# Optimization experiments

Hardware: AMD Instinct MI355X
Metric: run time of the kernel (lower is better)

## Reference

```python
import jax, jax.numpy as jnp
import numpy as np

T, D_ENC, H, D_EMB, VOCAB = 4000, 1024, 1024, 512, 8192
V = VOCAB + 1  # + blank
P = 800
TEMPERATURE = 1.0


def setup_inputs() -> dict:
    key = jax.random.key(0)
    ks = jax.random.split(key, 8)
    s = lambda d: 1.0 / np.sqrt(d)
    return {
        'enc_out': jax.random.normal(ks[0], (T, D_ENC), jnp.float32),
        'embedding': jax.random.normal(ks[1], (V, D_EMB), jnp.float32) * s(D_EMB),
        'W_ih': jax.random.normal(ks[2], (4 * H, D_EMB), jnp.float32) * s(D_EMB),
        'W_hh': jax.random.normal(ks[3], (4 * H, H), jnp.float32) * s(H),
        'b_lstm': jnp.zeros((4 * H,), jnp.float32),
        'W_pred': jax.random.normal(ks[4], (D_ENC, H), jnp.float32) * s(H),
        'b_pred': jnp.zeros((D_ENC,), jnp.float32),
        'W_join': jax.random.normal(ks[5], (V, D_ENC), jnp.float32) * s(D_ENC),
        'b_join': jnp.zeros((V,), jnp.float32),
        'phonemes': jax.random.randint(ks[6], (P,), 0, VOCAB, jnp.int32),
    }


def reference(enc_out, embedding, W_ih, W_hh, b_lstm, W_pred, b_pred, W_join, b_join, phonemes):
    blank_idx = embedding.shape[0] - 1
    n_phon = phonemes.shape[0]

    def predict_step(tok, h, c):
        # one-token RNNT predictor: embed -> LSTM cell -> projection to joiner dim
        x = embedding[tok]
        gates = x @ W_ih.T + h @ W_hh.T + b_lstm  # [4H]
        i, f, g, o = jnp.split(gates, 4)
        i, f, o = jax.nn.sigmoid(i), jax.nn.sigmoid(f), jax.nn.sigmoid(o)
        c2 = f * c + i * jnp.tanh(g)
        h2 = o * jnp.tanh(c2)
        pred = h2 @ W_pred.T + b_pred  # [D_ENC]
        return pred, h2, c2

    def step(carry, enc_t):
        tok, h, c, tp = carry
        pred, h2, c2 = predict_step(tok, h, c)
        logits = (jax.nn.relu(enc_t + pred) @ W_join.T + b_join) / TEMPERATURE
        logp = jax.nn.log_softmax(logits)  # [V]
        pick = jnp.argmax(logp)
        phon_done = tp >= n_phon
        is_blank = (pick == blank_idx) | phon_done
        next_phon = phonemes[jnp.minimum(tp, n_phon - 1)]
        prediction = jnp.where(is_blank, blank_idx, next_phon)
        # blank: keep hypothesis token/state; non-blank: advance to phoneme + new state
        tok2 = jnp.where(is_blank, tok, next_phon)
        h3 = jnp.where(is_blank, h, h2)
        c3 = jnp.where(is_blank, c, c2)
        tp2 = tp + jnp.where(is_blank, 0, 1)
        return (tok2, h3, c3, tp2), (logp, prediction, ~phon_done)

    # initial predictor pass with blank token from zero state (mirrors the warm-up predict call)
    h0 = jnp.zeros((W_hh.shape[1],), enc_out.dtype)
    c0 = jnp.zeros_like(h0)
    _, h_init, c_init = predict_step(jnp.int32(blank_idx), h0, c0)
    carry0 = (jnp.int32(blank_idx), h_init, c_init, jnp.int32(0))
    _, (alignment, predictions, valid) = jax.lax.scan(step, carry0, enc_out)
    return alignment, predictions, valid
```

## Files before the change

### kernel.cpp

```cpp
#include <hip/hip_runtime.h>
#include <math.h>

#define TT     4000
#define DENC   1024
#define HD     1024
#define DEMB   512
#define VD     8193
#define NPH    800
#define BLANK  8192
#define NWG    256
#define NTHR   512
#define CHUNK_M 800
#define NSTEP  (NPH + 2)
#define NSTEPP 802
#define NVT    65
#define NP     129
#define CHUNK  256

typedef __bf16 bf16x4 __attribute__((ext_vector_type(4)));
typedef __bf16 bf16x8 __attribute__((ext_vector_type(8)));
typedef float  f32x16 __attribute__((ext_vector_type(16)));

#define MEMSET_BYTES 20480
#define WSF_HX     1024
#define WSF_HHIST  5120
#define WSF_PREDS  826368
#define WSF_GXT    826368
#define WSF_PMAX   1646592
#define WSF_PSUM   2162592
#define WSF_PARG   2678592
#define WSF_LSE    3194592
#define WSF_AMAX   3198592
#define WSF_XBF    3199616
#define WSF_W16    4903552
#define WSF_END    9163392
#define NEED_MFMA  ((size_t)WSF_END * 4)
#define TST_IDX    512

#define L_HX     1024
#define L_HHIST  5120
#define L_PREDS  826368
#define F_PMAX 1646592
#define F_PSUM 1906592
#define F_PARG 2166592
#define F_LSE  2426592

#define GEMM_SMEM  12800
#define CHAIN_SMEM ((16 * NSTEPP + 2048 + 64) * 4)
#define JOIN_SMEM  (65536 + 128)
#define S_XH   0
#define S_GS   3072
#define S_C4   3088
#define S_TOK  3264
#define S_RED  4066
#define S_AMAX 4082
#define SMEM_FLOATS_F32 4352
#define SMEM_BYTES_F32 (SMEM_FLOATS_F32 * 4)


__device__ __forceinline__ float dot4(float4 a, float4 b, float acc) {
  acc = fmaf(a.x, b.x, acc); acc = fmaf(a.y, b.y, acc);
  acc = fmaf(a.z, b.z, acc); acc = fmaf(a.w, b.w, acc);
  return acc;
}
__device__ __forceinline__ float sigmf(float x) { return 1.f / (1.f + expf(-x)); }
__device__ __forceinline__ float sigm_fast(float x) { return 1.f / (1.f + __expf(-x)); }
__device__ __forceinline__ float tanh_fast(float x) {
  float e = __expf(2.f * x);
  return 1.f - 2.f / (e + 1.f);
}

__device__ __forceinline__ void combine3(float& m, float& s, int& am,
                                         float om, float os, int oa) {
  float mm = fmaxf(m, om);
  s = s * __expf(m - mm) + os * __expf(om - mm);
  if (om > m || (om == m && oa < am)) am = oa;
  m = mm;
}

__device__ __forceinline__ void gload16(const void* g, void* l) {
  __builtin_amdgcn_global_load_lds(
      (const __attribute__((address_space(1))) unsigned int*)g,
      (__attribute__((address_space(3))) unsigned int*)l, 16, 0, 0);
}

__device__ __forceinline__ float ld_coh(const float* p) {
  return __hip_atomic_load((const float*)p, __ATOMIC_RELAXED, __HIP_MEMORY_SCOPE_AGENT);
}

__device__ __forceinline__ void light_barrier(unsigned* flags, unsigned& ep) {
  unsigned* arrive  = flags;
  unsigned* release = flags + 256;
  __builtin_amdgcn_s_waitcnt(0);
  __syncthreads();
  if (blockIdx.x == 0) {
    int tid = threadIdx.x;
    if (tid > 0 && tid < NWG) {
      while (__hip_atomic_load(&arrive[tid], __ATOMIC_RELAXED, __HIP_MEMORY_SCOPE_AGENT) != ep) {}
    }
    __syncthreads();
    if (tid == 0)
      __hip_atomic_store(release, ep, __ATOMIC_RELAXED, __HIP_MEMORY_SCOPE_AGENT);
  } else {
    if (threadIdx.x == 0) {
      __hip_atomic_store(&arrive[blockIdx.x], ep, __ATOMIC_RELAXED, __HIP_MEMORY_SCOPE_AGENT);
      while (__hip_atomic_load(release, __ATOMIC_RELAXED, __HIP_MEMORY_SCOPE_AGENT) != ep) {}
    }
    __syncthreads();
  }
  asm volatile("" ::: "memory");
  ep++;
}

__device__ __forceinline__ void heavy_barrier(unsigned* flags) {
  unsigned* bar = flags + 257;
  __syncthreads();
  if (threadIdx.x == 0) {
    __threadfence();
    unsigned g = __hip_atomic_load(&bar[1], __ATOMIC_RELAXED, __HIP_MEMORY_SCOPE_AGENT);
    unsigned v = __hip_atomic_fetch_add(&bar[0], 1u, __ATOMIC_RELAXED, __HIP_MEMORY_SCOPE_AGENT);
    if (v == (unsigned)(NWG - 1)) {
      __hip_atomic_store(&bar[0], 0u, __ATOMIC_RELAXED, __HIP_MEMORY_SCOPE_AGENT);
      __hip_atomic_store(&bar[1], g + 1u, __ATOMIC_RELEASE, __HIP_MEMORY_SCOPE_AGENT);
    } else {
      while (__hip_atomic_load(&bar[1], __ATOMIC_RELAXED, __HIP_MEMORY_SCOPE_AGENT) == g)
        __builtin_amdgcn_s_sleep(1);
    }
    __threadfence();
  }
  __syncthreads();
}

__device__ void xbf_fill(const float* enc, const float* preds, __bf16* dst,
                         int t0, int K, int pi0, int g0, int gs) {
  int total = K << 8;
  for (int q = g0; q < total; q += gs) {
    int j = q >> 8, seg = q & 255;
    int pi = (pi0 < 0) ? NPH : pi0 + j;
    float4 e = ((const float4*)(enc + (size_t)(t0 + j) * 1024))[seg];
    float4 p = ((const float4*)(preds + (size_t)pi * 1024))[seg];
    bf16x4 r;
    r[0] = (__bf16)fmaxf(e.x + p.x, 0.f);
    r[1] = (__bf16)fmaxf(e.y + p.y, 0.f);
    r[2] = (__bf16)fmaxf(e.z + p.z, 0.f);
    r[3] = (__bf16)fmaxf(e.w + p.w, 0.f);
    *(bf16x4*)(dst + (size_t)j * 1024 + (seg << 2)) = r;
  }
}

__device__ void joiner_tiles(const __bf16* W16, const __bf16* xrows, const float* bj,
                             float* out_align, float* pmax, float* psum, int* parg,
                             char* smc, int t0, int K, int tile0, int tstride) {
  const int tid = threadIdx.x;
  const int wid = tid >> 6, lane = tid & 63;
  const int wj = wid & 3, wv = wid >> 2;
  const int l31 = lane & 31, lhi = lane >> 5;
  const int jt_n = (K + 127) >> 7;
  const int ntiles = jt_n * NVT;

  for (int tile = tile0; tile < ntiles; tile += tstride) {
    const int vt = tile % NVT, jt = tile / NVT;
    const int v0 = vt << 7, j0 = jt << 7;
    f32x16 acc0, acc1;
    #pragma unroll
    for (int i = 0; i < 16; ++i) { acc0[i] = 0.f; acc1[i] = 0.f; }

    auto stage = [&](int db, int kb) {
      char* wb = smc + db * 32768;
      char* xb = wb + 16384;
      #pragma unroll
      for (int p = 0; p < 2; ++p) {
        int sbase = p * 512 + wid * 64;
        int s = sbase + lane;
        int ks = s >> 7, r = s & 127;
        gload16(W16 + (size_t)(v0 + r) * 1024 + kb + ks * 8, wb + sbase * 16);
        gload16(xrows + (size_t)(j0 + r) * 1024 + kb + ks * 8, xb + sbase * 16);
      }
    };

    stage(0, 0);
    __syncthreads();
    int db = 0;
    for (int kb16 = 0; kb16 < 16; ++kb16) {
      if (kb16 < 15) stage(db ^ 1, (kb16 + 1) << 6);
      const char* wb = smc + db * 32768;
      const char* xb = wb + 16384;
      #pragma unroll
      for (int k16 = 0; k16 < 4; ++k16) {
        int ks = k16 * 2 + lhi;
        bf16x8 a  = *(const bf16x8*)(xb + ((ks << 7) + (wj << 5) + l31) * 16);
        bf16x8 b0 = *(const bf16x8*)(wb + ((ks << 7) + (wv << 6) + l31) * 16);
        bf16x8 b1 = *(const bf16x8*)(wb + ((ks << 7) + (wv << 6) + 32 + l31) * 16);
        acc0 = __builtin_amdgcn_mfma_f32_32x32x16_bf16(a, b0, acc0, 0, 0, 0);
        acc1 = __builtin_amdgcn_mfma_f32_32x32x16_bf16(a, b1, acc1, 0, 0, 0);
      }
      __syncthreads();
      db ^= 1;
    }

    const int v_0 = v0 + (wv << 6) + l31;
    const int v_1 = v_0 + 32;
    const float bj0 = (v_0 < VD) ? bj[v_0] : 0.f;
    const float bj1 = (v_1 < VD) ? bj[v_1] : 0.f;
    const int jbase = j0 + (wj << 5) + 4 * lhi;
    const bool npok = (v0 + (wv << 6)) < VD;
    const int np = (v0 >> 6) + wv;
    #pragma unroll
    for (int reg = 0; reg < 16; ++reg) {
      int j = jbase + (reg & 3) + 8 * (reg >> 2);
      bool jok = j < K;
      float lg0 = acc0[reg] + bj0;
      float lg1 = acc1[reg] + bj1;
      if (jok) {
        size_t ro = (size_t)(t0 + j) * VD;
        if (v_0 < VD) out_align[ro + v_0] = lg0;
        if (v_1 < VD) out_align[ro + v_1] = lg1;
      }
      float l0 = (v_0 < VD) ? lg0 : -1e30f;
      float l1 = (v_1 < VD) ? lg1 : -1e30f;
      float m = fmaxf(l0, l1);
      float ss = 0.f;
      if (v_0 < VD) ss += __expf(l0 - m);
      if (v_1 < VD) ss += __expf(l1 - m);
      int am = (l1 > l0) ? v_1 : v_0;
      #pragma unroll
      for (int msk = 1; msk <= 16; msk <<= 1) {
        float om = __shfl_xor(m, msk, 64);
        float os = __shfl_xor(ss, msk, 64);
        int oa = __shfl_xor(am, msk, 64);
        float mm = fmaxf(m, om);
        ss = ss * __expf(m - mm) + os * __expf(om - mm);
        if (om > m || (om == m && oa < am)) am = oa;
        m = mm;
      }
      if (l31 == 0 && jok && npok) {
        size_t pb = (size_t)(t0 + j) * NP + np;
        __hip_atomic_store(&pmax[pb], m, __ATOMIC_RELAXED, __HIP_MEMORY_SCOPE_AGENT);
        __hip_atomic_store(&psum[pb], ss, __ATOMIC_RELAXED, __HIP_MEMORY_SCOPE_AGENT);
        __hip_atomic_store(&parg[pb], am, __ATOMIC_RELAXED, __HIP_MEMORY_SCOPE_AGENT);
      }
    }
  }
}

__device__ __forceinline__ void merge_row129(const float* pmax, const float* psum,
                                             const int* parg, int row, int lane,
                                             float& m, float& s, int& am) {
  size_t b = (size_t)row * NP;
  m = ld_coh(pmax + b + lane);
  s = ld_coh(psum + b + lane);
  am = __hip_atomic_load(&parg[b + lane], __ATOMIC_RELAXED, __HIP_MEMORY_SCOPE_AGENT);
  {
    int i2 = lane + 64;
    float om = ld_coh(pmax + b + i2);
    float os = ld_coh(psum + b + i2);
    int oa = __hip_atomic_load(&parg[b + i2], __ATOMIC_RELAXED, __HIP_MEMORY_SCOPE_AGENT);
    combine3(m, s, am, om, os, oa);
  }
  if (lane == 0) {
    float om = ld_coh(pmax + b + 128);
    float os = ld_coh(psum + b + 128);
    int oa = __hip_atomic_load(&parg[b + 128], __ATOMIC_RELAXED, __HIP_MEMORY_SCOPE_AGENT);
    combine3(m, s, am, om, os, oa);
  }
  #pragma unroll
  for (int msk = 32; msk; msk >>= 1) {
    float om = __shfl_xor(m, msk, 64);
    float os = __shfl_xor(s, msk, 64);
    int oa = __shfl_xor(am, msk, 64);
    combine3(m, s, am, om, os, oa);
  }
}

__global__ __launch_bounds__(512) void wconv_kernel(const float* __restrict__ Wjoin,
                                                    float* wsf) {
  __bf16* w16 = (__bf16*)(wsf + WSF_W16);
  int g0 = blockIdx.x * 512 + threadIdx.x;
  int gs = gridDim.x * 512;
  for (int q = g0; q < VD * 256; q += gs) {
    int v = q >> 8, seg = q & 255;
    float4 w4 = ((const float4*)(Wjoin + (size_t)v * 1024))[seg];
    bf16x4 r;
    r[0] = (__bf16)w4.x; r[1] = (__bf16)w4.y; r[2] = (__bf16)w4.z; r[3] = (__bf16)w4.w;
    *(bf16x4*)(w16 + (size_t)v * 1024 + (seg << 2)) = r;
  }
}

__global__ __launch_bounds__(512) void gx_kernel(
    const float* __restrict__ Wih, const float* __restrict__ emb,
    const float* __restrict__ bl, const int* __restrict__ phon, float* wsf) {
  extern __shared__ float sm[];
  float* Wt = sm;
  float* Xt = sm + 2112;
  float* gxT = wsf + WSF_GXT;
  const int tid = threadIdx.x;
  const int tx = tid & 31, ty = tid >> 5;
  int ntiles = 32 * 13;
  for (int tile = blockIdx.x; tile < ntiles; tile += gridDim.x) {
    int vt = tile & 31, jt = tile >> 5;
    int v0 = vt * 128, j0 = jt * 64;
    float acc[4][4];
    #pragma unroll
    for (int a = 0; a < 4; ++a)
      #pragma unroll
      for (int q = 0; q < 4; ++q) acc[a][q] = 0.f;
    for (int kk = 0; kk < DEMB; kk += 16) {
      {
        int r = tid >> 2, seg = tid & 3;
        float4 wv = ((const float4*)(Wih + (size_t)(v0 + r) * DEMB + kk))[seg];
        Wt[(seg * 4 + 0) * 132 + r] = wv.x;
        Wt[(seg * 4 + 1) * 132 + r] = wv.y;
        Wt[(seg * 4 + 2) * 132 + r] = wv.z;
        Wt[(seg * 4 + 3) * 132 + r] = wv.w;
      }
      if (tid < 256) {
        int r = tid >> 2, seg = tid & 3;
        int j = j0 + r;
        float4 xv = make_float4(0.f, 0.f, 0.f, 0.f);
        if (j < NSTEP) {
          int tok = (j < 2) ? BLANK : phon[j - 2];
          xv = ((const float4*)(emb + (size_t)tok * DEMB + kk))[seg];
        }
        Xt[(seg * 4 + 0) * 68 + r] = xv.x;
        Xt[(seg * 4 + 1) * 68 + r] = xv.y;
        Xt[(seg * 4 + 2) * 68 + r] = xv.z;
        Xt[(seg * 4 + 3) * 68 + r] = xv.w;
      }
      __syncthreads();
      #pragma unroll
      for (int k = 0; k < 16; ++k) {
        float4 a = *(const float4*)(Wt + k * 132 + (tx << 2));
        float4 bq = *(const float4*)(Xt + k * 68 + (ty << 2));
        acc[0][0] = fmaf(a.x, bq.x, acc[0][0]); acc[1][0] = fmaf(a.y, bq.x, acc[1][0]);
        acc[2][0] = fmaf(a.z, bq.x, acc[2][0]); acc[3][0] = fmaf(a.w, bq.x, acc[3][0]);
        acc[0][1] = fmaf(a.x, bq.y, acc[0][1]); acc[1][1] = fmaf(a.y, bq.y, acc[1][1]);
        acc[2][1] = fmaf(a.z, bq.y, acc[2][1]); acc[3][1] = fmaf(a.w, bq.y, acc[3][1]);
        acc[0][2] = fmaf(a.x, bq.z, acc[0][2]); acc[1][2] = fmaf(a.y, bq.z, acc[1][2]);
        acc[2][2] = fmaf(a.z, bq.z, acc[2][2]); acc[3][2] = fmaf(a.w, bq.z, acc[3][2]);
        acc[0][3] = fmaf(a.x, bq.w, acc[0][3]); acc[1][3] = fmaf(a.y, bq.w, acc[1][3]);
        acc[2][3] = fmaf(a.z, bq.w, acc[2][3]); acc[3][3] = fmaf(a.w, bq.w, acc[3][3]);
      }
      __syncthreads();
    }
    int vb = v0 + (tx << 2), jb0 = j0 + (ty << 2);
    #pragma unroll
    for (int jj = 0; jj < 4; ++jj) {
      int j = jb0 + jj;
      if (j >= NSTEP) continue;
      #pragma unroll
      for (int q = 0; q < 4; ++q)
        gxT[(size_t)(vb + q) * NSTEPP + j] = acc[q][jj] + bl[vb + q];
    }
  }
}

__global__ __launch_bounds__(NTHR) void chain_kernel(const float* __restrict__ Whh,
                                                     float* wsf) {
  extern __shared__ float sm[];
  float* gxl = sm;
  float* hb  = sm + 16 * NSTEPP;
  float* GS  = hb + 2048;
  const int tid = threadIdx.x;
  const int w = tid >> 6, l = tid & 63;
  const int b = blockIdx.x;
  const float* gxT = wsf + WSF_GXT;
  float* hhist = wsf + WSF_HHIST;
  unsigned long long* hx = (unsigned long long*)(wsf + WSF_HX);

  float4 W0[4], W1[4];
  {
    int rr0 = 2 * w, rr1 = 2 * w + 1;
    int gr0 = ((rr0 >> 2) << 10) + 4 * b + (rr0 & 3);
    int gr1 = ((rr1 >> 2) << 10) + 4 * b + (rr1 & 3);
    const float4* h0 = (const float4*)(Whh + (size_t)gr0 * HD);
    const float4* h1 = (const float4*)(Whh + (size_t)gr1 * HD);
    #pragma unroll
    for (int i = 0; i < 4; ++i) { W0[i] = h0[l + 64 * i]; W1[i] = h1[l + 64 * i]; }
  }
  for (int rr = 0; rr < 16; ++rr) {
    int gr = ((rr >> 2) << 10) + 4 * b + (rr & 3);
    for (int s = tid; s < NSTEP; s += NTHR)
      gxl[rr * NSTEPP + s] = gxT[(size_t)gr * NSTEPP + s];
  }
  for (int i = tid; i < 1024; i += NTHR) hb[i] = 0.f;
  __syncthreads();

  float c_reg = 0.f;
  for (int s = 0; s < NSTEP; ++s) {
    int p = s & 1;
    const float4* h4 = (const float4*)(hb + p * 1024);
    float a0 = 0.f, a1 = 0.f;
    #pragma unroll
    for (int i = 0; i < 4; ++i) {
      float4 hv = h4[l + 64 * i];
      a0 = dot4(W0[i], hv, a0);
      a1 = dot4(W1[i], hv, a1);
    }
    #pragma unroll
    for (int m = 32; m; m >>= 1) {
      a0 += __shfl_xor(a0, m, 64);
      a1 += __shfl_xor(a1, m, 64);
    }
    if (l == 0) { GS[2 * w] = a0; GS[2 * w + 1] = a1; }
    __syncthreads();
    if (tid < 4) {
      int j = tid;
      float gi = GS[j]      + gxl[j * NSTEPP + s];
      float gf = GS[4 + j]  + gxl[(4 + j) * NSTEPP + s];
      float gg = GS[8 + j]  + gxl[(8 + j) * NSTEPP + s];
      float go = GS[12 + j] + gxl[(12 + j) * NSTEPP + s];
      float c2 = sigm_fast(gf) * c_reg + sigm_fast(gi) * tanh_fast(gg);
      float h2 = sigm_fast(go) * tanh_fast(c2);
      c_reg = c2;
      int cell = 4 * b + j;
      unsigned long long pk = ((unsigned long long)(unsigned)(s + 1) << 32)
                            | (unsigned long long)__float_as_uint(h2);
      __hip_atomic_store(&hx[(p ^ 1) * 1024 + cell], pk,
                         __ATOMIC_RELAXED, __HIP_MEMORY_SCOPE_AGENT);
      hhist[(size_t)s * HD + cell] = h2;
    }
    if (s + 1 < NSTEP) {
      unsigned tg = (unsigned)(s + 1);
      const unsigned long long* src = hx + (p ^ 1) * 1024;
      unsigned long long v0, v1;
      do {
        v0 = __hip_atomic_load(&src[2 * tid],     __ATOMIC_RELAXED, __HIP_MEMORY_SCOPE_AGENT);
        v1 = __hip_atomic_load(&src[2 * tid + 1], __ATOMIC_RELAXED, __HIP_MEMORY_SCOPE_AGENT);
      } while ((unsigned)(v0 >> 32) != tg || (unsigned)(v1 >> 32) != tg);
      float* dst = hb + (p ^ 1) * 1024 + 2 * tid;
      dst[0] = __uint_as_float((unsigned)v0);
      dst[1] = __uint_as_float((unsigned)v1);
    }
    __syncthreads();
  }
}

__global__ __launch_bounds__(512) void preds_kernel(
    const float* __restrict__ Wpred, const float* __restrict__ bp, float* wsf) {
  extern __shared__ float sm[];
  float* Wt = sm;
  float* Xt = sm + 2112;
  const float* hhist = wsf + WSF_HHIST;
  float* preds = wsf + WSF_PREDS;
  const int tid = threadIdx.x;
  const int tx = tid & 31, ty = tid >> 5;
  int ntiles = 8 * 13;
  for (int tile = blockIdx.x; tile < ntiles; tile += gridDim.x) {
    int vt = tile & 7, jt = tile >> 3;
    int v0 = vt * 128, j0 = jt * 64;
    float acc[4][4];
    #pragma unroll
    for (int a = 0; a < 4; ++a)
      #pragma unroll
      for (int q = 0; q < 4; ++q) acc[a][q] = 0.f;
    for (int kk = 0; kk < 1024; kk += 16) {
      {
        int r = tid >> 2, seg = tid & 3;
        float4 wv = ((const float4*)(Wpred + (size_t)(v0 + r) * HD + kk))[seg];
        Wt[(seg * 4 + 0) * 132 + r] = wv.x;
        Wt[(seg * 4 + 1) * 132 + r] = wv.y;
        Wt[(seg * 4 + 2) * 132 + r] = wv.z;
        Wt[(seg * 4 + 3) * 132 + r] = wv.w;
      }
      if (tid < 256) {
        int r = tid >> 2, seg = tid & 3;
        int j = j0 + r;
        float4 xv = make_float4(0.f, 0.f, 0.f, 0.f);
        if (j <= NPH) xv = ((const float4*)(hhist + (size_t)(j + 1) * HD + kk))[seg];
        Xt[(seg * 4 + 0) * 68 + r] = xv.x;
        Xt[(seg * 4 + 1) * 68 + r] = xv.y;
        Xt[(seg * 4 + 2) * 68 + r] = xv.z;
        Xt[(seg * 4 + 3) * 68 + r] = xv.w;
      }
      __syncthreads();
      #pragma unroll
      for (int k = 0; k < 16; ++k) {
        float4 a = *(const float4*)(Wt + k * 132 + (tx << 2));
        float4 bq = *(const float4*)(Xt + k * 68 + (ty << 2));
        acc[0][0] = fmaf(a.x, bq.x, acc[0][0]); acc[1][0] = fmaf(a.y, bq.x, acc[1][0]);
        acc[2][0] = fmaf(a.z, bq.x, acc[2][0]); acc[3][0] = fmaf(a.w, bq.x, acc[3][0]);
        acc[0][1] = fmaf(a.x, bq.y, acc[0][1]); acc[1][1] = fmaf(a.y, bq.y, acc[1][1]);
        acc[2][1] = fmaf(a.z, bq.y, acc[2][1]); acc[3][1] = fmaf(a.w, bq.y, acc[3][1]);
        acc[0][2] = fmaf(a.x, bq.z, acc[0][2]); acc[1][2] = fmaf(a.y, bq.z, acc[1][2]);
        acc[2][2] = fmaf(a.z, bq.z, acc[2][2]); acc[3][2] = fmaf(a.w, bq.z, acc[3][2]);
        acc[0][3] = fmaf(a.x, bq.w, acc[0][3]); acc[1][3] = fmaf(a.y, bq.w, acc[1][3]);
        acc[2][3] = fmaf(a.z, bq.w, acc[2][3]); acc[3][3] = fmaf(a.w, bq.w, acc[3][3]);
      }
      __syncthreads();
    }
    int vb = v0 + (tx << 2), jb0 = j0 + (ty << 2);
    #pragma unroll
    for (int jj = 0; jj < 4; ++jj) {
      int j = jb0 + jj;
      if (j > NPH) continue;
      #pragma unroll
      for (int q = 0; q < 4; ++q)
        preds[(size_t)j * 1024 + vb + q] = acc[q][jj] + bp[vb + q];
    }
  }
}

__global__ void xspec_kernel(const float* __restrict__ enc, float* wsf) {
  xbf_fill(enc, wsf + WSF_PREDS, (__bf16*)(wsf + WSF_XBF), 0, CHUNK_M, 0,
           blockIdx.x * blockDim.x + threadIdx.x, gridDim.x * blockDim.x);
}

__global__ __launch_bounds__(NTHR) void joinspec_kernel(const float* __restrict__ bj,
                                                        float* out, float* wsf) {
  extern __shared__ float sm[];
  joiner_tiles((__bf16*)(wsf + WSF_W16), (__bf16*)(wsf + WSF_XBF), bj, out,
               wsf + WSF_PMAX, wsf + WSF_PSUM, (int*)(wsf + WSF_PARG),
               (char*)sm, 0, CHUNK_M, blockIdx.x, gridDim.x);
}

__global__ __launch_bounds__(NTHR) void decode_coop(
    const float* enc, const float* bj, const int* phon, float* out, float* wsf) {
  extern __shared__ float sm[];
  char* smc = (char*)sm;
  unsigned* flags = (unsigned*)wsf;
  float* preds = wsf + WSF_PREDS;
  float* pmax = wsf + WSF_PMAX;
  float* psum = wsf + WSF_PSUM;
  int* parg = (int*)(wsf + WSF_PARG);
  float* lse = wsf + WSF_LSE;
  int* amaxws = (int*)(wsf + WSF_AMAX);
  __bf16* xbf = (__bf16*)(wsf + WSF_XBF);
  __bf16* w16 = (__bf16*)(wsf + WSF_W16);
  float* out_pred  = out + (size_t)TT * VD;
  float* out_valid = out + (size_t)TT * VD + TT;

  const int tid = threadIdx.x;
  const int wid = tid >> 6, lane = tid & 63;
  unsigned ep = 1;
  int t = 0, tp = 0, iter = 0;

  while (t < TT && tp < NPH) {
    int K = CHUNK_M;
    if (TT - t < K) K = TT - t;
    if (NPH - tp < K) K = NPH - tp;
    if (iter > 0) {
      heavy_barrier(flags);
      xbf_fill(enc, preds, xbf, t, K, tp, blockIdx.x * NTHR + tid, gridDim.x * NTHR);
      heavy_barrier(flags);
      joiner_tiles(w16, xbf, bj, out, pmax, psum, parg, smc, t, K,
                   blockIdx.x, gridDim.x);
    }
    light_barrier(flags, ep);
    for (int j = blockIdx.x * 8 + wid; j < K; j += gridDim.x * 8) {
      float m, s; int am;
      merge_row129(pmax, psum, parg, t + j, lane, m, s, am);
      if (lane == 0) {
        __hip_atomic_store(&amaxws[j], am, __ATOMIC_RELAXED, __HIP_MEMORY_SCOPE_AGENT);
        lse[t + j] = m + logf(s);
      }
    }
    light_barrier(flags, ep);
    int cand = K;
    for (int idx = tid; idx < K; idx += NTHR) {
      int a = __hip_atomic_load(&amaxws[idx], __ATOMIC_RELAXED, __HIP_MEMORY_SCOPE_AGENT);
      if (a == BLANK && idx < cand) cand = idx;
    }
    #pragma unroll
    for (int msk = 32; msk; msk >>= 1) cand = min(cand, __shfl_xor(cand, msk, 64));
    int* red = (int*)(smc + 65536);
    if (lane == 0) red[wid] = cand;
    __syncthreads();
    if (tid == 0) {
      int mn = red[0];
      for (int w2 = 1; w2 < 8; ++w2) mn = min(mn, red[w2]);
      red[8] = mn;
    }
    __syncthreads();
    int jb = red[8];
    __syncthreads();
    int nacc = (jb < K) ? jb + 1 : K;
    int nadv = (jb < K) ? jb : K;
    if (blockIdx.x == 0) {
      for (int j = tid; j < nacc; j += NTHR) {
        out_pred[t + j] = (j == jb) ? (float)BLANK : (float)phon[tp + j];
        out_valid[t + j] = 1.f;
      }
    }
    t += nacc; tp += nadv; ++iter;
  }

  if (t < TT) {
    xbf_fill(enc, preds, xbf + (size_t)(t - 800) * 1024, t, TT - t, -1,
             blockIdx.x * NTHR + tid, gridDim.x * NTHR);
  }
  if (blockIdx.x == 0 && tid == 0) ((int*)wsf)[TST_IDX] = t;
}

__global__ __launch_bounds__(NTHR) void jointail_kernel(const float* __restrict__ bj,
                                                        float* out, float* wsf) {
  extern __shared__ float sm[];
  int t = ((const int*)wsf)[TST_IDX];
  if (t >= TT) return;
  joiner_tiles((__bf16*)(wsf + WSF_W16),
               (__bf16*)(wsf + WSF_XBF) + (size_t)(t - 800) * 1024, bj, out,
               wsf + WSF_PMAX, wsf + WSF_PSUM, (int*)(wsf + WSF_PARG),
               (char*)sm, t, TT - t, blockIdx.x, gridDim.x);
}

__global__ __launch_bounds__(NTHR) void mergetail_kernel(float* out, float* wsf) {
  int t = ((const int*)wsf)[TST_IDX];
  float* lse = wsf + WSF_LSE;
  float* out_pred  = out + (size_t)TT * VD;
  float* out_valid = out + (size_t)TT * VD + TT;
  const int wid = threadIdx.x >> 6, lane = threadIdx.x & 63;
  for (int row = t + blockIdx.x * 8 + wid; row < TT; row += gridDim.x * 8) {
    float m, s; int am;
    merge_row129(wsf + WSF_PMAX, wsf + WSF_PSUM, (const int*)(wsf + WSF_PARG),
                 row, lane, m, s, am);
    if (lane == 0) {
      lse[row] = m + logf(s);
      out_pred[row] = (float)BLANK;
      out_valid[row] = 0.f;
    }
  }
}

__global__ __launch_bounds__(256) void sub_kernel(float* out, const float* wsf) {
  const float* lse = wsf + WSF_LSE;
  for (int row = blockIdx.x; row < TT; row += gridDim.x) {
    float l = lse[row];
    float4* p4 = (float4*)(out + (size_t)row * VD);
    #pragma unroll
    for (int k = 0; k < 8; ++k) {
      int i = threadIdx.x + k * 256;
      float4 v = p4[i];
      v.x -= l; v.y -= l; v.z -= l; v.w -= l;
      p4[i] = v;
    }
    if (threadIdx.x == 0) out[(size_t)row * VD + 8192] -= l;
  }
}

struct Ctx {
  const float *enc, *emb, *Wih, *Whh, *bl, *Wpred, *bp, *Wjoin, *bj;
  const int* phon;
  unsigned long long* hx;
  float *hhist, *preds, *pmax, *psum, *lse;
  int* parg;
  unsigned* flags;
  float *out_align, *out_pred, *out_valid;
};

__device__ void chain_all_legacy(const Ctx& C, float* sm) {
  const int tid = threadIdx.x;
  const int w = tid >> 6, l = tid & 63;
  const int b = blockIdx.x;
  int* tok_sm = (int*)(sm + S_TOK);
  for (int s = tid; s < NSTEP; s += NTHR)
    tok_sm[s] = (s < 2) ? BLANK : C.phon[s - 2];
  float4 W0[6], W1[6];
  {
    int rr0 = 2 * w, rr1 = 2 * w + 1;
    int gr0 = ((rr0 >> 2) << 10) + 4 * b + (rr0 & 3);
    int gr1 = ((rr1 >> 2) << 10) + 4 * b + (rr1 & 3);
    const float4* ih0 = (const float4*)(C.Wih + (size_t)gr0 * DEMB);
    const float4* hh0 = (const float4*)(C.Whh + (size_t)gr0 * HD);
    const float4* ih1 = (const float4*)(C.Wih + (size_t)gr1 * DEMB);
    const float4* hh1 = (const float4*)(C.Whh + (size_t)gr1 * HD);
    W0[0] = ih0[l];       W0[1] = ih0[64 + l];
    W0[2] = hh0[l];       W0[3] = hh0[64 + l];
    W0[4] = hh0[128 + l]; W0[5] = hh0[192 + l];
    W1[0] = ih1[l];       W1[1] = ih1[64 + l];
    W1[2] = hh1[l];       W1[3] = hh1[64 + l];
    W1[4] = hh1[128 + l]; W1[5] = hh1[192 + l];
  }
  float bi = 0.f, bf = 0.f, bg = 0.f, bo = 0.f;
  if (tid < 4) {
    bi = C.bl[4 * b + tid];
    bf = C.bl[1024 + 4 * b + tid];
    bg = C.bl[2048 + 4 * b + tid];
    bo = C.bl[3072 + 4 * b + tid];
    sm[S_C4 + tid] = 0.f;
  }
  for (int i = tid; i < 1536; i += NTHR) sm[S_XH + i] = 0.f;
  if (tid < 512) sm[S_XH + tid] = C.emb[(size_t)BLANK * DEMB + tid];
  __syncthreads();
  unsigned long long* hx = C.hx;
  for (int s = 0; s < NSTEP; ++s) {
    int p = s & 1;
    const float4* xh4 = (const float4*)(sm + S_XH + p * 1536);
    float a0 = 0.f, a1 = 0.f;
    #pragma unroll
    for (int i = 0; i < 6; ++i) {
      float4 v = xh4[i * 64 + l];
      a0 = dot4(W0[i], v, a0);
      a1 = dot4(W1[i], v, a1);
    }
    #pragma unroll
    for (int m = 32; m; m >>= 1) {
      a0 += __shfl_xor(a0, m, 64);
      a1 += __shfl_xor(a1, m, 64);
    }
    if (l == 0) { sm[S_GS + 2 * w] = a0; sm[S_GS + 2 * w + 1] = a1; }
    if (s + 1 < NSTEP && tid < 512)
      sm[S_XH + (1 - p) * 1536 + tid] = C.emb[(size_t)tok_sm[s + 1] * DEMB + tid];
    __syncthreads();
    if (tid < 4) {
      int j = tid;
      float gi = sm[S_GS + j]      + bi;
      float gf = sm[S_GS + 4 + j]  + bf;
      float gg = sm[S_GS + 8 + j]  + bg;
      float go = sm[S_GS + 12 + j] + bo;
      float cc = sm[S_C4 + j];
      float c2 = sigmf(gf) * cc + sigmf(gi) * tanhf(gg);
      float h2 = sigmf(go) * tanhf(c2);
      sm[S_C4 + j] = c2;
      int cell = 4 * b + j;
      C.hhist[(size_t)s * HD + cell] = h2;
      unsigned long long pk = ((unsigned long long)(unsigned)(s + 1) << 32)
                            | (unsigned long long)__float_as_uint(h2);
      __hip_atomic_store(&hx[(1 - p) * 1024 + cell], pk,
                         __ATOMIC_RELAXED, __HIP_MEMORY_SCOPE_AGENT);
    }
    if (s + 1 < NSTEP) {
      unsigned tg = (unsigned)(s + 1);
      #pragma unroll
      for (int kq = 0; kq < 2; ++kq) {
        int k = tid + kq * 512;
        unsigned long long v;
        do {
          v = __hip_atomic_load(&hx[(1 - p) * 1024 + k],
                                __ATOMIC_RELAXED, __HIP_MEMORY_SCOPE_AGENT);
        } while ((unsigned)(v >> 32) != tg);
        sm[S_XH + (1 - p) * 1536 + 512 + k] = __uint_as_float((unsigned)v);
      }
    }
    __syncthreads();
  }
}

__device__ void preds_gemm_legacy(const Ctx& C, float* sm) {
  float* Wt = sm;
  float* Xt = sm + 2112;
  const int tid = threadIdx.x;
  const int tx = tid & 31, ty = tid >> 5;
  int ntiles = 8 * 13;
  for (int tile = blockIdx.x; tile < ntiles; tile += NWG) {
    int vt = tile & 7, jt = tile >> 3;
    int v0 = vt * 128, j0 = jt * 64;
    float acc[4][4];
    #pragma unroll
    for (int a = 0; a < 4; ++a)
      #pragma unroll
      for (int q = 0; q < 4; ++q) acc[a][q] = 0.f;
    for (int kk = 0; kk < 1024; kk += 16) {
      {
        int r = tid >> 2, seg = tid & 3;
        float4 wv = ((const float4*)(C.Wpred + (size_t)(v0 + r) * HD + kk))[seg];
        Wt[(seg * 4 + 0) * 132 + r] = wv.x;
        Wt[(seg * 4 + 1) * 132 + r] = wv.y;
        Wt[(seg * 4 + 2) * 132 + r] = wv.z;
        Wt[(seg * 4 + 3) * 132 + r] = wv.w;
      }
      if (tid < 256) {
        int r = tid >> 2, seg = tid & 3;
        int j = j0 + r;
        float4 xv = make_float4(0.f, 0.f, 0.f, 0.f);
        if (j <= NPH) xv = ((const float4*)(C.hhist + (size_t)(j + 1) * HD + kk))[seg];
        Xt[(seg * 4 + 0) * 68 + r] = xv.x;
        Xt[(seg * 4 + 1) * 68 + r] = xv.y;
        Xt[(seg * 4 + 2) * 68 + r] = xv.z;
        Xt[(seg * 4 + 3) * 68 + r] = xv.w;
      }
      __syncthreads();
      #pragma unroll
      for (int k = 0; k < 16; ++k) {
        float4 a = *(const float4*)(Wt + k * 132 + (tx << 2));
        float4 bq = *(const float4*)(Xt + k * 68 + (ty << 2));
        acc[0][0] = fmaf(a.x, bq.x, acc[0][0]); acc[1][0] = fmaf(a.y, bq.x, acc[1][0]);
        acc[2][0] = fmaf(a.z, bq.x, acc[2][0]); acc[3][0] = fmaf(a.w, bq.x, acc[3][0]);
        acc[0][1] = fmaf(a.x, bq.y, acc[0][1]); acc[1][1] = fmaf(a.y, bq.y, acc[1][1]);
        acc[2][1] = fmaf(a.z, bq.y, acc[2][1]); acc[3][1] = fmaf(a.w, bq.y, acc[3][1]);
        acc[0][2] = fmaf(a.x, bq.z, acc[0][2]); acc[1][2] = fmaf(a.y, bq.z, acc[1][2]);
        acc[2][2] = fmaf(a.z, bq.z, acc[2][2]); acc[3][2] = fmaf(a.w, bq.z, acc[3][2]);
        acc[0][3] = fmaf(a.x, bq.w, acc[0][3]); acc[1][3] = fmaf(a.y, bq.w, acc[1][3]);
        acc[2][3] = fmaf(a.z, bq.w, acc[2][3]); acc[3][3] = fmaf(a.w, bq.w, acc[3][3]);
      }
      __syncthreads();
    }
    int vb = v0 + (tx << 2), jb0 = j0 + (ty << 2);
    #pragma unroll
    for (int jj = 0; jj < 4; ++jj) {
      int j = jb0 + jj;
      if (j > NPH) continue;
      #pragma unroll
      for (int q = 0; q < 4; ++q)
        C.preds[(size_t)j * 1024 + vb + q] = acc[q][jj] + C.bp[vb + q];
    }
  }
}

__device__ void joiner_gemm_f32(const Ctx& C, float* sm, int t0, int K, int pi0) {
  float* Wt = sm;
  float* Xt = sm + 2112;
  const int tid = threadIdx.x;
  const int tx = tid & 31, ty = tid >> 5;
  int jt_n = (K + 63) >> 6;
  int ntiles = jt_n * NVT;
  for (int tile = blockIdx.x; tile < ntiles; tile += NWG) {
    int vt = tile % NVT, jt = tile / NVT;
    int v0 = vt * 128, j0 = jt * 64;
    float acc[4][4];
    #pragma unroll
    for (int a = 0; a < 4; ++a)
      #pragma unroll
      for (int q = 0; q < 4; ++q) acc[a][q] = 0.f;
    for (int kk = 0; kk < 1024; kk += 16) {
      {
        int r = tid >> 2, seg = tid & 3;
        int v = v0 + r;
        float4 wv = make_float4(0.f, 0.f, 0.f, 0.f);
        if (v < VD) wv = ((const float4*)(C.Wjoin + (size_t)v * 1024 + kk))[seg];
        Wt[(seg * 4 + 0) * 132 + r] = wv.x;
        Wt[(seg * 4 + 1) * 132 + r] = wv.y;
        Wt[(seg * 4 + 2) * 132 + r] = wv.z;
        Wt[(seg * 4 + 3) * 132 + r] = wv.w;
      }
      if (tid < 256) {
        int r = tid >> 2, seg = tid & 3;
        int j = j0 + r;
        float4 xv = make_float4(0.f, 0.f, 0.f, 0.f);
        if (j < K) {
          int pi = (pi0 < 0) ? NPH : (pi0 + j);
          float4 e = ((const float4*)(C.enc + (size_t)(t0 + j) * DENC + kk))[seg];
          float4 pr = ((const float4*)(C.preds + (size_t)pi * 1024 + kk))[seg];
          xv.x = fmaxf(e.x + pr.x, 0.f);
          xv.y = fmaxf(e.y + pr.y, 0.f);
          xv.z = fmaxf(e.z + pr.z, 0.f);
          xv.w = fmaxf(e.w + pr.w, 0.f);
        }
        Xt[(seg * 4 + 0) * 68 + r] = xv.x;
        Xt[(seg * 4 + 1) * 68 + r] = xv.y;
        Xt[(seg * 4 + 2) * 68 + r] = xv.z;
        Xt[(seg * 4 + 3) * 68 + r] = xv.w;
      }
      __syncthreads();
      #pragma unroll
      for (int k = 0; k < 16; ++k) {
        float4 a = *(const float4*)(Wt + k * 132 + (tx << 2));
        float4 bq = *(const float4*)(Xt + k * 68 + (ty << 2));
        acc[0][0] = fmaf(a.x, bq.x, acc[0][0]); acc[1][0] = fmaf(a.y, bq.x, acc[1][0]);
        acc[2][0] = fmaf(a.z, bq.x, acc[2][0]); acc[3][0] = fmaf(a.w, bq.x, acc[3][0]);
        acc[0][1] = fmaf(a.x, bq.y, acc[0][1]); acc[1][1] = fmaf(a.y, bq.y, acc[1][1]);
        acc[2][1] = fmaf(a.z, bq.y, acc[2][1]); acc[3][1] = fmaf(a.w, bq.y, acc[3][1]);
        acc[0][2] = fmaf(a.x, bq.z, acc[0][2]); acc[1][2] = fmaf(a.y, bq.z, acc[1][2]);
        acc[2][2] = fmaf(a.z, bq.z, acc[2][2]); acc[3][2] = fmaf(a.w, bq.z, acc[3][2]);
        acc[0][3] = fmaf(a.x, bq.w, acc[0][3]); acc[1][3] = fmaf(a.y, bq.w, acc[1][3]);
        acc[2][3] = fmaf(a.z, bq.w, acc[2][3]); acc[3][3] = fmaf(a.w, bq.w, acc[3][3]);
      }
      __syncthreads();
    }
    int vb = v0 + (tx << 2);
    int jb0 = j0 + (ty << 2);
    float bjv[4];
    #pragma unroll
    for (int q = 0; q < 4; ++q) bjv[q] = (vb + q < VD) ? C.bj[vb + q] : 0.f;
    #pragma unroll
    for (int jj = 0; jj < 4; ++jj) {
      int j = jb0 + jj;
      if (j >= K) continue;
      size_t ro = (size_t)(t0 + j) * VD;
      float lg[4];
      float m = -1e30f; int am = vb;
      #pragma unroll
      for (int q = 0; q < 4; ++q) {
        int v = vb + q;
        if (v < VD) {
          lg[q] = acc[q][jj] + bjv[q];
          C.out_align[ro + v] = lg[q];
          if (lg[q] > m) { m = lg[q]; am = v; }
        } else lg[q] = -1e30f;
      }
      float ss = 0.f;
      #pragma unroll
      for (int q = 0; q < 4; ++q)
        if (vb + q < VD) ss += __expf(lg[q] - m);
      #pragma unroll
      for (int msk = 16; msk; msk >>= 1) {
        float om = __shfl_xor(m, msk, 64);
        float os = __shfl_xor(ss, msk, 64);
        int oa = __shfl_xor(am, msk, 64);
        combine3(m, ss, am, om, os, oa);
      }
      if (tx == 0) {
        size_t pb = (size_t)(t0 + j) * NVT + vt;
        __hip_atomic_store(&C.pmax[pb], m, __ATOMIC_RELAXED, __HIP_MEMORY_SCOPE_AGENT);
        __hip_atomic_store(&C.psum[pb], ss, __ATOMIC_RELAXED, __HIP_MEMORY_SCOPE_AGENT);
        __hip_atomic_store(&C.parg[pb], am, __ATOMIC_RELAXED, __HIP_MEMORY_SCOPE_AGENT);
      }
    }
  }
}

__device__ __forceinline__ void merge_row65(const Ctx& C, int row, int lane,
                                            float& m, float& s, int& am) {
  size_t b = (size_t)row * NVT;
  m = ld_coh(C.pmax + b + lane);
  s = ld_coh(C.psum + b + lane);
  am = __hip_atomic_load(&C.parg[b + lane], __ATOMIC_RELAXED, __HIP_MEMORY_SCOPE_AGENT);
  if (lane == 0) {
    float om = ld_coh(C.pmax + b + 64);
    float os = ld_coh(C.psum + b + 64);
    int oa = __hip_atomic_load(&C.parg[b + 64], __ATOMIC_RELAXED, __HIP_MEMORY_SCOPE_AGENT);
    combine3(m, s, am, om, os, oa);
  }
  #pragma unroll
  for (int msk = 32; msk; msk >>= 1) {
    float om = __shfl_xor(m, msk, 64);
    float os = __shfl_xor(s, msk, 64);
    int oa = __shfl_xor(am, msk, 64);
    combine3(m, s, am, om, os, oa);
  }
}

__global__ __launch_bounds__(NTHR) void decode_kernel_f32(
    const float* enc, const float* emb, const float* Wih, const float* Whh,
    const float* bl, const float* Wpred, const float* bp, const float* Wjoin,
    const float* bj, const int* phon, float* out, float* wsf) {
  extern __shared__ float sm[];
  Ctx C;
  C.enc = enc; C.emb = emb; C.Wih = Wih; C.Whh = Whh; C.bl = bl;
  C.Wpred = Wpred; C.bp = bp; C.Wjoin = Wjoin; C.bj = bj; C.phon = phon;
  C.flags = (unsigned*)wsf;
  C.hx = (unsigned long long*)(wsf + L_HX);
  C.hhist = wsf + L_HHIST;
  C.preds = wsf + L_PREDS;
  C.pmax = wsf + F_PMAX;
  C.psum = wsf + F_PSUM;
  C.parg = (int*)(wsf + F_PARG);
  C.lse = wsf + F_LSE;
  C.out_align = out;
  C.out_pred  = out + (size_t)TT * VD;
  C.out_valid = out + (size_t)TT * VD + TT;

  const int tid = threadIdx.x;
  const int wid = tid >> 6, lane = tid & 63;
  unsigned ep = 1;

  chain_all_legacy(C, sm);
  heavy_barrier(C.flags);
  preds_gemm_legacy(C, sm);
  heavy_barrier(C.flags);

  int t = 0, tp = 0;
  while (t < TT && tp < NPH) {
    int K = CHUNK;
    if (TT - t < K) K = TT - t;
    if (NPH - tp < K) K = NPH - tp;
    joiner_gemm_f32(C, sm, t, K, tp);
    light_barrier(C.flags, ep);
    int* amax_l = (int*)(sm + S_AMAX);
    for (int j = wid; j < K; j += 8) {
      float m, s; int am;
      merge_row65(C, t + j, lane, m, s, am);
      if (lane == 0) {
        amax_l[j] = am;
        C.lse[t + j] = m + logf(s);
      }
    }
    __syncthreads();
    int cand = K;
    if (tid < K && amax_l[tid] == BLANK) cand = tid;
    #pragma unroll
    for (int msk = 32; msk; msk >>= 1) cand = min(cand, __shfl_xor(cand, msk, 64));
    int* red = (int*)(sm + S_RED);
    if (lane == 0) red[wid] = cand;
    __syncthreads();
    if (tid == 0) {
      int mn = red[0];
      for (int w2 = 1; w2 < 8; ++w2) mn = min(mn, red[w2]);
      red[8] = mn;
    }
    __syncthreads();
    int jb = red[8];
    __syncthreads();
    int nacc = (jb < K) ? jb + 1 : K;
    int nadv = (jb < K) ? jb : K;
    if (blockIdx.x == 0) {
      int* tok_sm = (int*)(sm + S_TOK);
      for (int j = tid; j < nacc; j += NTHR) {
        C.out_pred[t + j] = (j == jb) ? (float)BLANK : (float)tok_sm[tp + j + 2];
        C.out_valid[t + j] = 1.f;
      }
    }
    t += nacc; tp += nadv;
    if (jb < K) heavy_barrier(C.flags);
  }
  if (t < TT) {
    int Kt = TT - t;
    joiner_gemm_f32(C, sm, t, Kt, -1);
    light_barrier(C.flags, ep);
    for (int i = blockIdx.x * 8 + wid; i < Kt; i += NWG * 8) {
      float m, s; int am;
      merge_row65(C, t + i, lane, m, s, am);
      if (lane == 0) C.lse[t + i] = m + logf(s);
    }
    const int gtid = blockIdx.x * NTHR + tid;
    for (int i = gtid; i < Kt; i += NWG * NTHR) {
      C.out_pred[t + i] = (float)BLANK;
      C.out_valid[t + i] = 0.f;
    }
  }
  heavy_barrier(C.flags);
  for (int row = blockIdx.x; row < TT; row += NWG) {
    float l = C.lse[row];
    float* p = C.out_align + (size_t)row * VD;
    for (int i = tid; i < VD; i += NTHR) p[i] -= l;
  }
}


extern "C" void kernel_launch(void* const* d_in, const int* in_sizes, int n_in,
                              void* d_out, int out_size, void* d_ws, size_t ws_size,
                              hipStream_t stream) {
  const float* enc   = (const float*)d_in[0];
  const float* emb   = (const float*)d_in[1];
  const float* Wih   = (const float*)d_in[2];
  const float* Whh   = (const float*)d_in[3];
  const float* bl    = (const float*)d_in[4];
  const float* Wpred = (const float*)d_in[5];
  const float* bp    = (const float*)d_in[6];
  const float* Wjoin = (const float*)d_in[7];
  const float* bj    = (const float*)d_in[8];
  const int*   phon  = (const int*)d_in[9];
  float* out = (float*)d_out;
  float* wsf = (float*)d_ws;

  hipMemsetAsync(d_ws, 0, MEMSET_BYTES, stream);

  if (ws_size >= NEED_MFMA) {
    hipFuncSetAttribute((const void*)chain_kernel,
                        hipFuncAttributeMaxDynamicSharedMemorySize, CHAIN_SMEM);
    hipFuncSetAttribute((const void*)joinspec_kernel,
                        hipFuncAttributeMaxDynamicSharedMemorySize, JOIN_SMEM);
    hipFuncSetAttribute((const void*)decode_coop,
                        hipFuncAttributeMaxDynamicSharedMemorySize, JOIN_SMEM);
    hipFuncSetAttribute((const void*)jointail_kernel,
                        hipFuncAttributeMaxDynamicSharedMemorySize, JOIN_SMEM);

    wconv_kernel<<<1024, 512, 0, stream>>>(Wjoin, wsf);
    gx_kernel<<<416, 512, GEMM_SMEM, stream>>>(Wih, emb, bl, phon, wsf);
    {
      const float* WhhA = Whh; float* wsfA = wsf;
      void* a2[] = { &WhhA, &wsfA };
      hipError_t e = hipLaunchCooperativeKernel((void*)chain_kernel, dim3(256), dim3(NTHR),
                                                a2, CHAIN_SMEM, stream);
      if (e != hipSuccess)
        chain_kernel<<<dim3(256), dim3(NTHR), CHAIN_SMEM, stream>>>(Whh, wsf);
    }
    preds_kernel<<<104, 512, GEMM_SMEM, stream>>>(Wpred, bp, wsf);
    xspec_kernel<<<1024, 256, 0, stream>>>(enc, wsf);
    joinspec_kernel<<<455, NTHR, JOIN_SMEM, stream>>>(bj, out, wsf);
    {
      const float* encA = enc; const float* bjA = bj; const int* phonA = phon;
      float* outA = out; float* wsfA = wsf;
      void* a3[] = { &encA, &bjA, &phonA, &outA, &wsfA };
      hipError_t e = hipLaunchCooperativeKernel((void*)decode_coop, dim3(NWG), dim3(NTHR),
                                                a3, JOIN_SMEM, stream);
      if (e != hipSuccess)
        decode_coop<<<dim3(NWG), dim3(NTHR), JOIN_SMEM, stream>>>(enc, bj, phon, out, wsf);
    }
    jointail_kernel<<<1664, NTHR, JOIN_SMEM, stream>>>(bj, out, wsf);
    mergetail_kernel<<<256, NTHR, 0, stream>>>(out, wsf);
    sub_kernel<<<2048, 256, 0, stream>>>(out, wsf);
  } else {
    hipFuncSetAttribute((const void*)decode_kernel_f32,
                        hipFuncAttributeMaxDynamicSharedMemorySize, SMEM_BYTES_F32);
    void* args[] = { &enc, &emb, &Wih, &Whh, &bl, &Wpred, &bp, &Wjoin, &bj, &phon, &out, &wsf };
    hipError_t e = hipLaunchCooperativeKernel((void*)decode_kernel_f32, dim3(NWG), dim3(NTHR),
                                              args, SMEM_BYTES_F32, stream);
    if (e != hipSuccess) {
      decode_kernel_f32<<<dim3(NWG), dim3(NTHR), SMEM_BYTES_F32, stream>>>(
          enc, emb, Wih, Whh, bl, Wpred, bp, Wjoin, bj, phon, out, wsf);
    }
  }
}
```

Baseline: 2.683 ms.

## Pack LSTM hidden exchange as bf16 pairs and merge prep kernels

The recurrent chain kernel now publishes each hidden value as a 16-bit tag plus a bf16 value, and pairs of cells are packed into one 64-bit atomic word. Each polling thread therefore spins on a single load instead of two, which halves the inter-workgroup exchange traffic on the serial critical path. Separately, the Wjoin bf16 conversion and the gx GEMM are merged into one launch with disjoint block ranges. The packing rounds the recurrent h to bf16, which adds precision loss that feeds back through every LSTM step. The 16-bit step tag only works because the step count stays below 65536.

```diff
diff --git a/kernel.cpp b/kernel.cpp
--- a/kernel.cpp
+++ b/kernel.cpp
@@ -20,6 +20,7 @@
 typedef __bf16 bf16x4 __attribute__((ext_vector_type(4)));
 typedef __bf16 bf16x8 __attribute__((ext_vector_type(8)));
 typedef float  f32x16 __attribute__((ext_vector_type(16)));
+typedef unsigned long long u64t;
 
 #define MEMSET_BYTES 20480
 #define WSF_HX     1024
@@ -69,6 +70,9 @@
   float e = __expf(2.f * x);
   return 1.f - 2.f / (e + 1.f);
 }
+__device__ __forceinline__ float bfbits_to_f32(unsigned u16v) {
+  return __builtin_bit_cast(float, (u16v & 0xFFFFu) << 16);
+}
 
 __device__ __forceinline__ void combine3(float& m, float& s, int& am,
                                          float om, float os, int oa) {
@@ -272,31 +276,31 @@
   }
 }
 
-__global__ __launch_bounds__(512) void wconv_kernel(const float* __restrict__ Wjoin,
-                                                    float* wsf) {
-  __bf16* w16 = (__bf16*)(wsf + WSF_W16);
-  int g0 = blockIdx.x * 512 + threadIdx.x;
-  int gs = gridDim.x * 512;
-  for (int q = g0; q < VD * 256; q += gs) {
-    int v = q >> 8, seg = q & 255;
-    float4 w4 = ((const float4*)(Wjoin + (size_t)v * 1024))[seg];
-    bf16x4 r;
-    r[0] = (__bf16)w4.x; r[1] = (__bf16)w4.y; r[2] = (__bf16)w4.z; r[3] = (__bf16)w4.w;
-    *(bf16x4*)(w16 + (size_t)v * 1024 + (seg << 2)) = r;
-  }
-}
-
-__global__ __launch_bounds__(512) void gx_kernel(
+__global__ __launch_bounds__(512) void prep_kernel(
     const float* __restrict__ Wih, const float* __restrict__ emb,
-    const float* __restrict__ bl, const int* __restrict__ phon, float* wsf) {
+    const float* __restrict__ bl, const int* __restrict__ phon,
+    const float* __restrict__ Wjoin, float* wsf) {
   extern __shared__ float sm[];
+  const int tid = threadIdx.x;
+  if (blockIdx.x >= 416) {
+    __bf16* w16 = (__bf16*)(wsf + WSF_W16);
+    int g0 = (blockIdx.x - 416) * 512 + tid;
+    int gs = 1024 * 512;
+    for (int q = g0; q < VD * 256; q += gs) {
+      int v = q >> 8, seg = q & 255;
+      float4 w4 = ((const float4*)(Wjoin + (size_t)v * 1024))[seg];
+      bf16x4 r;
+      r[0] = (__bf16)w4.x; r[1] = (__bf16)w4.y; r[2] = (__bf16)w4.z; r[3] = (__bf16)w4.w;
+      *(bf16x4*)(w16 + (size_t)v * 1024 + (seg << 2)) = r;
+    }
+    return;
+  }
   float* Wt = sm;
   float* Xt = sm + 2112;
   float* gxT = wsf + WSF_GXT;
-  const int tid = threadIdx.x;
   const int tx = tid & 31, ty = tid >> 5;
   int ntiles = 32 * 13;
-  for (int tile = blockIdx.x; tile < ntiles; tile += gridDim.x) {
+  for (int tile = blockIdx.x; tile < ntiles; tile += 416) {
     int vt = tile & 31, jt = tile >> 5;
     int v0 = vt * 128, j0 = jt * 64;
     float acc[4][4];
@@ -365,7 +369,7 @@
   const int b = blockIdx.x;
   const float* gxT = wsf + WSF_GXT;
   float* hhist = wsf + WSF_HHIST;
-  unsigned long long* hx = (unsigned long long*)(wsf + WSF_HX);
+  u64t* hx = (u64t*)(wsf + WSF_HX);
 
   float4 W0[4], W1[4];
   {
@@ -413,23 +417,26 @@
       float h2 = sigm_fast(go) * tanh_fast(c2);
       c_reg = c2;
       int cell = 4 * b + j;
-      unsigned long long pk = ((unsigned long long)(unsigned)(s + 1) << 32)
-                            | (unsigned long long)__float_as_uint(h2);
-      __hip_atomic_store(&hx[(p ^ 1) * 1024 + cell], pk,
-                         __ATOMIC_RELAXED, __HIP_MEMORY_SCOPE_AGENT);
+      unsigned hb16 = (unsigned)__builtin_bit_cast(unsigned short, (__bf16)h2);
+      unsigned pk = (((unsigned)(s + 1)) << 16) | hb16;
+      unsigned other = __shfl_xor(pk, 1, 64);
+      if ((tid & 1) == 0) {
+        u64t pk2 = (u64t)pk | ((u64t)other << 32);
+        __hip_atomic_store(&hx[((p ^ 1) << 9) + (cell >> 1)], pk2,
+                           __ATOMIC_RELAXED, __HIP_MEMORY_SCOPE_AGENT);
+      }
       hhist[(size_t)s * HD + cell] = h2;
     }
     if (s + 1 < NSTEP) {
       unsigned tg = (unsigned)(s + 1);
-      const unsigned long long* src = hx + (p ^ 1) * 1024;
-      unsigned long long v0, v1;
+      const u64t* src = hx + ((p ^ 1) << 9);
+      u64t v;
       do {
-        v0 = __hip_atomic_load(&src[2 * tid],     __ATOMIC_RELAXED, __HIP_MEMORY_SCOPE_AGENT);
-        v1 = __hip_atomic_load(&src[2 * tid + 1], __ATOMIC_RELAXED, __HIP_MEMORY_SCOPE_AGENT);
-      } while ((unsigned)(v0 >> 32) != tg || (unsigned)(v1 >> 32) != tg);
+        v = __hip_atomic_load(&src[tid], __ATOMIC_RELAXED, __HIP_MEMORY_SCOPE_AGENT);
+      } while (((unsigned)(v >> 16) & 0xFFFFu) != tg || (unsigned)(v >> 48) != tg);
       float* dst = hb + (p ^ 1) * 1024 + 2 * tid;
-      dst[0] = __uint_as_float((unsigned)v0);
-      dst[1] = __uint_as_float((unsigned)v1);
+      dst[0] = bfbits_to_f32((unsigned)v);
+      dst[1] = bfbits_to_f32((unsigned)(v >> 32));
     }
     __syncthreads();
   }
@@ -1043,8 +1050,7 @@
     hipFuncSetAttribute((const void*)jointail_kernel,
                         hipFuncAttributeMaxDynamicSharedMemorySize, JOIN_SMEM);
 
-    wconv_kernel<<<1024, 512, 0, stream>>>(Wjoin, wsf);
-    gx_kernel<<<416, 512, GEMM_SMEM, stream>>>(Wih, emb, bl, phon, wsf);
+    prep_kernel<<<1440, 512, GEMM_SMEM, stream>>>(Wih, emb, bl, phon, Wjoin, wsf);
     {
       const float* WhhA = Whh; float* wsfA = wsf;
       void* a2[] = { &WhhA, &wsfA };
```

Result: slower. 2.890 ms (+7.7%).
